# Optimization experiments

Measured on AMD Instinct MI355X. Metric: run time of the kernel, lower is better.

The kernel has to match this reference:

```python
import jax, jax.numpy as jnp
import numpy as np


def setup_inputs() -> dict:
    key = jax.random.key(0)
    k1, k2, k3, k4 = jax.random.split(key, 4)
    return {
        "hidden_states": jax.random.normal(k1, (9, 16, 2048, 768), dtype=jnp.float32),
        "input_ids": jax.random.randint(k2, (16, 2048), 0, 512),
        "layer_logits": jax.random.normal(k3, (8,), dtype=jnp.float32) * 0.02,
        "W": jax.random.normal(k4, (4, 768), dtype=jnp.float32) * 0.02,
        "hte_token_id": 5,
        "d_token_ids": jnp.arange(3),
        "window": 4,
    }


def reference(hidden_states, input_ids, layer_logits, W, hte_token_id, d_token_ids, window):
    # hidden_states: (L+1, B, T, H); drop the embedding layer like the torch code
    layers = hidden_states[1:]              # (L, B, T, H)
    L, B, T, H = layers.shape
    C = W.shape[0]                          # num_heads
    ids = input_ids                         # (B, T)
    wl = jax.nn.softmax(layer_logits)       # (L,) layer mixture weights

    def masked_pool(sel, mask):
        # sel: (L, B, P, H), mask: (B, P) valid-token mask
        scores = jnp.einsum('lbph,ch->lbpc', sel, W)
        scores = jnp.where(mask[None, :, :, None], scores, -jnp.inf)
        attn = jax.nn.softmax(scores, axis=2)          # softmax over tokens P
        pooled = jnp.einsum('lbph,lbpc->lbch', sel, attn)
        return jnp.einsum('l,lbch->bch', wl, pooled).reshape(B, C * H)

    # --- HTE window pooling: first occurrence of hte_token_id, window tokens after ---
    is_hte = ids == hte_token_id
    pos = jnp.where(is_hte.any(axis=1), jnp.argmax(is_hte, axis=1), T - 1)  # (B,)
    offs = jnp.arange(window + 1)
    widx = pos[:, None] + offs              # (B, window+1)
    wvalid = widx < T
    widx = jnp.clip(widx, 0, T - 1)
    sel = layers[:, jnp.arange(B)[:, None], widx]      # (L, B, window+1, H)
    hte_feat = masked_pool(sel, wvalid)

    # --- descriptor pooling: all positions whose id is in d_token_ids ---
    # (masked softmax over full T is math-identical to index_select + softmax,
    #  since softmax-weighted sum is permutation invariant and masked weights are 0)
    dmask = jnp.isin(ids, d_token_ids)      # (B, T)
    dmask = jnp.where(dmask.any(axis=1)[:, None], dmask, jnp.arange(T)[None, :] == 0)
    desc_feat = masked_pool(layers, dmask)

    return jnp.concatenate([hte_feat, desc_feat], axis=-1)  # (B, 2*C*H)
```

## Files before the change

kernel.cpp:

```cpp
#include <hip/hip_runtime.h>
#include <hip/hip_bf16.h>
#include <math.h>


#define CMAX 8
#define KMAX 4

__global__ void mha_scan(const int* __restrict__ ids, const int* __restrict__ hte_id_p,
                         const int* __restrict__ dtok, int nD, int T,
                         int* __restrict__ pos_out, int* __restrict__ nd_out,
                         int* __restrict__ dlist) {
    int b = blockIdx.x;
    __shared__ int s_pos, s_cnt;
    if (threadIdx.x == 0) { s_pos = 0x7fffffff; s_cnt = 0; }
    __syncthreads();
    const int hte = hte_id_p[0];
    const int* row = ids + (size_t)b * T;
    for (int t = threadIdx.x; t < T; t += blockDim.x) {
        int id = row[t];
        if (id == hte) atomicMin(&s_pos, t);
        bool isd = false;
        for (int j = 0; j < nD; ++j) isd |= (id == dtok[j]);
        if (isd) {
            int slot = atomicAdd(&s_cnt, 1);
            dlist[(size_t)b * T + slot] = t;
        }
    }
    __syncthreads();
    if (threadIdx.x == 0) {
        pos_out[b] = (s_pos == 0x7fffffff) ? (T - 1) : s_pos;
        if (s_cnt == 0) { dlist[(size_t)b * T] = 0; nd_out[b] = 1; }
        else nd_out[b] = s_cnt;
    }
}

__global__ void mha_pool(const float* __restrict__ hs, const float* __restrict__ logits,
                         const float* __restrict__ W, const int* __restrict__ win_p,
                         const int* __restrict__ pos_in, const int* __restrict__ nd_in,
                         const int* __restrict__ dlist,
                         int L, int B, int T, int H, int C,
                         float* __restrict__ partial) {
    extern __shared__ float smem[];
    float* lds_W   = smem;
    float* lds_sc  = lds_W + (size_t)C * H;
    float* lds_ms  = lds_sc + (size_t)T * C;
    int*   lds_pos = (int*)(lds_ms + 2 * C);

    const int bx   = blockIdx.x;
    const int part = bx / (L * B);
    const int rem  = bx % (L * B);
    const int l    = rem / B;
    const int b    = rem % B;
    const int tid  = threadIdx.x;
    const int lane = tid & 63;
    const int wave = tid >> 6;
    const int nwaves = blockDim.x >> 6;

    for (int i = tid; i < C * H; i += blockDim.x) lds_W[i] = W[i];

    int npos, p0 = 0;
    if (part == 0) {
        npos = win_p[0] + 1;
        p0 = pos_in[b];
        for (int p = tid; p < npos; p += blockDim.x) {
            int t = p0 + p;
            lds_pos[p] = (t < T) ? t : (T - 1);
        }
    } else {
        npos = nd_in[b];
        for (int p = tid; p < npos; p += blockDim.x)
            lds_pos[p] = dlist[(size_t)b * T + p];
    }
    __syncthreads();

    const float* base = hs + ((size_t)(l + 1) * B + b) * (size_t)T * H;

    for (int p = wave; p < npos; p += nwaves) {
        int t = lds_pos[p];
        bool valid = (part != 0) || (p0 + p < T);
        const float* v = base + (size_t)t * H;
        float s[CMAX];
        #pragma unroll
        for (int c = 0; c < CMAX; ++c) s[c] = 0.f;
        for (int h = lane; h < H; h += 64) {
            float x = v[h];
            for (int c = 0; c < C; ++c) s[c] += x * lds_W[c * H + h];
        }
        for (int c = 0; c < C; ++c) {
            float r = s[c];
            for (int off = 32; off > 0; off >>= 1) r += __shfl_down(r, off);
            if (lane == 0) lds_sc[p * C + c] = valid ? r : -1e30f;
        }
    }
    __syncthreads();

    for (int c = wave; c < C; c += nwaves) {
        float m = -1e30f;
        for (int p = lane; p < npos; p += 64) m = fmaxf(m, lds_sc[p * C + c]);
        for (int off = 32; off > 0; off >>= 1) m = fmaxf(m, __shfl_xor(m, off));
        float sum = 0.f;
        for (int p = lane; p < npos; p += 64) sum += expf(lds_sc[p * C + c] - m);
        for (int off = 32; off > 0; off >>= 1) sum += __shfl_xor(sum, off);
        if (lane == 0) { lds_ms[c] = m; lds_ms[C + c] = sum; }
    }
    __syncthreads();
    for (int i = tid; i < npos * C; i += blockDim.x) {
        int c = i % C;
        lds_sc[i] = expf(lds_sc[i] - lds_ms[c]) / lds_ms[C + c];
    }
    __syncthreads();

    const int K = (H + blockDim.x - 1) / blockDim.x;
    float acc[CMAX][KMAX];
    #pragma unroll
    for (int c = 0; c < CMAX; ++c)
        #pragma unroll
        for (int k = 0; k < KMAX; ++k) acc[c][k] = 0.f;

    for (int p = 0; p < npos; ++p) {
        int t = lds_pos[p];
        const float* v = base + (size_t)t * H;
        float a[CMAX];
        for (int c = 0; c < C; ++c) a[c] = lds_sc[p * C + c];
        for (int k = 0; k < K; ++k) {
            int h = tid + k * blockDim.x;
            if (h < H) {
                float x = v[h];
                for (int c = 0; c < C; ++c) acc[c][k] += a[c] * x;
            }
        }
    }

    float mL = -1e30f;
    for (int i = 0; i < L; ++i) mL = fmaxf(mL, logits[i]);
    float sL = 0.f;
    for (int i = 0; i < L; ++i) sL += expf(logits[i] - mL);
    float wl = expf(logits[l] - mL) / sL;

    float* outp = partial + ((size_t)(part * L + l) * B + b) * ((size_t)C * H);
    for (int k = 0; k < K; ++k) {
        int h = tid + k * blockDim.x;
        if (h < H)
            for (int c = 0; c < C; ++c) outp[c * H + h] = wl * acc[c][k];
    }
}

__global__ void mha_combine(const float* __restrict__ partial, float* __restrict__ out,
                            int L, int B, int CH, int n) {
    int idx = blockIdx.x * blockDim.x + threadIdx.x;
    if (idx >= n) return;
    int b    = idx / (2 * CH);
    int r    = idx % (2 * CH);
    int part = r / CH;
    int ch   = r % CH;
    float s = 0.f;
    for (int l = 0; l < L; ++l)
        s += partial[((size_t)(part * L + l) * B + b) * (size_t)CH + ch];
    out[idx] = s;
}

extern "C" void kernel_launch(void* const* d_in, const int* in_sizes, int n_in,
                              void* d_out, int out_size, void* d_ws, size_t ws_size,
                              hipStream_t stream) {
    const float* hs     = (const float*)d_in[0];
    const int*   ids    = (const int*)d_in[1];
    const float* logits = (const float*)d_in[2];
    const float* W      = (const float*)d_in[3];
    const int*   hte_id = (const int*)d_in[4];
    const int*   dtok   = (const int*)d_in[5];
    const int*   win    = (const int*)d_in[6];

    const int L  = in_sizes[2];
    const int CH = in_sizes[3];
    const int BT = in_sizes[1];
    const int B  = out_size / (2 * CH);
    const int T  = BT / B;
    const long long total = (long long)in_sizes[0];
    const int H  = (int)(total / ((long long)(L + 1) * BT));
    const int C  = CH / H;
    const int nD = in_sizes[5];

    char* ws = (char*)d_ws;
    int* pos   = (int*)ws;
    int* nd    = pos + B;
    int* dlist = nd + B;
    uintptr_t poff = (uintptr_t)(dlist + (size_t)B * T);
    poff = (poff + 15) & ~(uintptr_t)15;
    float* partial = (float*)poff;

    mha_scan<<<B, 256, 0, stream>>>(ids, hte_id, dtok, nD, T, pos, nd, dlist);

    size_t smem = ((size_t)C * H + (size_t)T * C + 2 * C) * sizeof(float)
                + (size_t)T * sizeof(int);
    mha_pool<<<2 * L * B, 256, smem, stream>>>(hs, logits, W, win, pos, nd, dlist,
                                               L, B, T, H, C, partial);

    mha_combine<<<(out_size + 255) / 256, 256, 0, stream>>>(partial, (float*)d_out,
                                                            L, B, CH, out_size);
}
```

Before: 1.048 ms.

## Fuse token scan and layer combine into templated pooling kernel with atomics

Removes the separate scan kernel by having each pooling block rescan its batch row of token ids into LDS. It also drops the combine kernel: each block atomically adds its layer-weighted result into a pre-zeroed output. The score loop now uses float4 loads, and C and K are compile-time template parameters so loops fully unroll. In exchange, every block redundantly scans the ids row, and float atomics make the summation order nondeterministic.

```diff
diff --git a/kernel.cpp b/kernel.cpp
--- a/kernel.cpp
+++ b/kernel.cpp
@@ -6,45 +6,24 @@
 #define CMAX 8
 #define KMAX 4
 
-__global__ void mha_scan(const int* __restrict__ ids, const int* __restrict__ hte_id_p,
-                         const int* __restrict__ dtok, int nD, int T,
-                         int* __restrict__ pos_out, int* __restrict__ nd_out,
-                         int* __restrict__ dlist) {
-    int b = blockIdx.x;
-    __shared__ int s_pos, s_cnt;
-    if (threadIdx.x == 0) { s_pos = 0x7fffffff; s_cnt = 0; }
-    __syncthreads();
-    const int hte = hte_id_p[0];
-    const int* row = ids + (size_t)b * T;
-    for (int t = threadIdx.x; t < T; t += blockDim.x) {
-        int id = row[t];
-        if (id == hte) atomicMin(&s_pos, t);
-        bool isd = false;
-        for (int j = 0; j < nD; ++j) isd |= (id == dtok[j]);
-        if (isd) {
-            int slot = atomicAdd(&s_cnt, 1);
-            dlist[(size_t)b * T + slot] = t;
-        }
-    }
-    __syncthreads();
-    if (threadIdx.x == 0) {
-        pos_out[b] = (s_pos == 0x7fffffff) ? (T - 1) : s_pos;
-        if (s_cnt == 0) { dlist[(size_t)b * T] = 0; nd_out[b] = 1; }
-        else nd_out[b] = s_cnt;
-    }
+__global__ void mha_zero(float* __restrict__ out, int n) {
+    int i = blockIdx.x * blockDim.x + threadIdx.x;
+    if (i < n) out[i] = 0.f;
 }
 
-__global__ void mha_pool(const float* __restrict__ hs, const float* __restrict__ logits,
-                         const float* __restrict__ W, const int* __restrict__ win_p,
-                         const int* __restrict__ pos_in, const int* __restrict__ nd_in,
-                         const int* __restrict__ dlist,
-                         int L, int B, int T, int H, int C,
-                         float* __restrict__ partial) {
+template <int C, int K>
+__global__ void mha_fused(const float* __restrict__ hs, const float* __restrict__ logits,
+                          const float* __restrict__ W, const int* __restrict__ ids,
+                          const int* __restrict__ hte_p, const int* __restrict__ dtok,
+                          int nD, const int* __restrict__ win_p,
+                          int L, int B, int T, int H,
+                          float* __restrict__ out) {
     extern __shared__ float smem[];
     float* lds_W   = smem;
     float* lds_sc  = lds_W + (size_t)C * H;
     float* lds_ms  = lds_sc + (size_t)T * C;
     int*   lds_pos = (int*)(lds_ms + 2 * C);
+    __shared__ int s_pos, s_cnt;
 
     const int bx   = blockIdx.x;
     const int part = bx / (L * B);
@@ -56,39 +35,63 @@
     const int wave = tid >> 6;
     const int nwaves = blockDim.x >> 6;
 
+    if (tid == 0) { s_pos = 0x7fffffff; s_cnt = 0; }
     for (int i = tid; i < C * H; i += blockDim.x) lds_W[i] = W[i];
+    __syncthreads();
+
+    const int hte = hte_p[0];
+    const int* row = ids + (size_t)b * T;
+    for (int t = tid; t < T; t += blockDim.x) {
+        int id = row[t];
+        if (id == hte) atomicMin(&s_pos, t);
+        if (part == 1) {
+            bool isd = false;
+            for (int j = 0; j < nD; ++j) isd |= (id == dtok[j]);
+            if (isd) {
+                int slot = atomicAdd(&s_cnt, 1);
+                lds_pos[slot] = t;
+            }
+        }
+    }
+    __syncthreads();
 
     int npos, p0 = 0;
     if (part == 0) {
         npos = win_p[0] + 1;
-        p0 = pos_in[b];
+        p0 = (s_pos == 0x7fffffff) ? (T - 1) : s_pos;
         for (int p = tid; p < npos; p += blockDim.x) {
             int t = p0 + p;
             lds_pos[p] = (t < T) ? t : (T - 1);
         }
     } else {
-        npos = nd_in[b];
-        for (int p = tid; p < npos; p += blockDim.x)
-            lds_pos[p] = dlist[(size_t)b * T + p];
+        npos = s_cnt;
+        if (npos == 0) { if (tid == 0) lds_pos[0] = 0; npos = 1; }
     }
     __syncthreads();
 
     const float* base = hs + ((size_t)(l + 1) * B + b) * (size_t)T * H;
 
+    const int H4 = H >> 2;
+    const float4* lds_W4 = (const float4*)lds_W;
     for (int p = wave; p < npos; p += nwaves) {
         int t = lds_pos[p];
         bool valid = (part != 0) || (p0 + p < T);
-        const float* v = base + (size_t)t * H;
-        float s[CMAX];
-        #pragma unroll
-        for (int c = 0; c < CMAX; ++c) s[c] = 0.f;
-        for (int h = lane; h < H; h += 64) {
-            float x = v[h];
-            for (int c = 0; c < C; ++c) s[c] += x * lds_W[c * H + h];
-        }
+        const float4* v = (const float4*)(base + (size_t)t * H);
+        float s[C];
+        #pragma unroll
+        for (int c = 0; c < C; ++c) s[c] = 0.f;
+        for (int i = lane; i < H4; i += 64) {
+            float4 x = v[i];
+            #pragma unroll
+            for (int c = 0; c < C; ++c) {
+                float4 w = lds_W4[c * H4 + i];
+                s[c] += x.x * w.x + x.y * w.y + x.z * w.z + x.w * w.w;
+            }
+        }
+        #pragma unroll
         for (int c = 0; c < C; ++c) {
             float r = s[c];
-            for (int off = 32; off > 0; off >>= 1) r += __shfl_down(r, off);
+            for (int off = 32; off > 0; off >>= 1) r += __shfl_xor(r, off);
             if (lane == 0) lds_sc[p * C + c] = valid ? r : -1e30f;
         }
     }
@@ -110,22 +113,24 @@
     }
     __syncthreads();
 
-    const int K = (H + blockDim.x - 1) / blockDim.x;
-    float acc[CMAX][KMAX];
+    float acc[C][K];
     #pragma unroll
-    for (int c = 0; c < CMAX; ++c)
-        #pragma unroll
-        for (int k = 0; k < KMAX; ++k) acc[c][k] = 0.f;
+    for (int c = 0; c < C; ++c)
+        #pragma unroll
+        for (int k = 0; k < K; ++k) acc[c][k] = 0.f;
 
     for (int p = 0; p < npos; ++p) {
         int t = lds_pos[p];
         const float* v = base + (size_t)t * H;
-        float a[CMAX];
+        float a[C];
+        #pragma unroll
         for (int c = 0; c < C; ++c) a[c] = lds_sc[p * C + c];
+        #pragma unroll
         for (int k = 0; k < K; ++k) {
             int h = tid + k * blockDim.x;
             if (h < H) {
                 float x = v[h];
+                #pragma unroll
                 for (int c = 0; c < C; ++c) acc[c][k] += a[c] * x;
             }
         }
@@ -137,26 +142,118 @@
     for (int i = 0; i < L; ++i) sL += expf(logits[i] - mL);
     float wl = expf(logits[l] - mL) / sL;
 
-    float* outp = partial + ((size_t)(part * L + l) * B + b) * ((size_t)C * H);
+    float* outp = out + (size_t)b * (2 * C * H) + (size_t)part * C * H;
+    #pragma unroll
     for (int k = 0; k < K; ++k) {
         int h = tid + k * blockDim.x;
         if (h < H)
-            for (int c = 0; c < C; ++c) outp[c * H + h] = wl * acc[c][k];
+            #pragma unroll
+            for (int c = 0; c < C; ++c)
+                atomicAdd(&outp[c * H + h], wl * acc[c][k]);
     }
 }
 
-__global__ void mha_combine(const float* __restrict__ partial, float* __restrict__ out,
-                            int L, int B, int CH, int n) {
-    int idx = blockIdx.x * blockDim.x + threadIdx.x;
-    if (idx >= n) return;
-    int b    = idx / (2 * CH);
-    int r    = idx % (2 * CH);
-    int part = r / CH;
-    int ch   = r % CH;
-    float s = 0.f;
-    for (int l = 0; l < L; ++l)
-        s += partial[((size_t)(part * L + l) * B + b) * (size_t)CH + ch];
-    out[idx] = s;
+__global__ void mha_fused_gen(const float* __restrict__ hs, const float* __restrict__ logits,
+                              const float* __restrict__ W, const int* __restrict__ ids,
+                              const int* __restrict__ hte_p, const int* __restrict__ dtok,
+                              int nD, const int* __restrict__ win_p,
+                              int L, int B, int T, int H, int C,
+                              float* __restrict__ out) {
+    extern __shared__ float smem[];
+    float* lds_W   = smem;
+    float* lds_sc  = lds_W + (size_t)C * H;
+    float* lds_ms  = lds_sc + (size_t)T * C;
+    int*   lds_pos = (int*)(lds_ms + 2 * C);
+    __shared__ int s_pos, s_cnt;
+
+    const int bx   = blockIdx.x;
+    const int part = bx / (L * B);
+    const int rem  = bx % (L * B);
+    const int l    = rem / B;
+    const int b    = rem % B;
+    const int tid  = threadIdx.x;
+    const int lane = tid & 63;
+    const int wave = tid >> 6;
+    const int nwaves = blockDim.x >> 6;
+
+    if (tid == 0) { s_pos = 0x7fffffff; s_cnt = 0; }
+    for (int i = tid; i < C * H; i += blockDim.x) lds_W[i] = W[i];
+    __syncthreads();
+
+    const int hte = hte_p[0];
+    const int* row = ids + (size_t)b * T;
+    for (int t = tid; t < T; t += blockDim.x) {
+        int id = row[t];
+        if (id == hte) atomicMin(&s_pos, t);
+        if (part == 1) {
+            bool isd = false;
+            for (int j = 0; j < nD; ++j) isd |= (id == dtok[j]);
+            if (isd) lds_pos[atomicAdd(&s_cnt, 1)] = t;
+        }
+    }
+    __syncthreads();
+
+    int npos, p0 = 0;
+    if (part == 0) {
+        npos = win_p[0] + 1;
+        p0 = (s_pos == 0x7fffffff) ? (T - 1) : s_pos;
+        for (int p = tid; p < npos; p += blockDim.x) {
+            int t = p0 + p;
+            lds_pos[p] = (t < T) ? t : (T - 1);
+        }
+    } else {
+        npos = s_cnt;
+        if (npos == 0) { if (tid == 0) lds_pos[0] = 0; npos = 1; }
+    }
+    __syncthreads();
+
+    const float* base = hs + ((size_t)(l + 1) * B + b) * (size_t)T * H;
+
+    for (int pc = wave * C; pc < npos * C; pc += nwaves * C) {
+        int p = pc / C;
+        int t = lds_pos[p];
+        bool valid = (part != 0) || (p0 + p < T);
+        const float* v = base + (size_t)t * H;
+        for (int c = 0; c < C; ++c) {
+            float s = 0.f;
+            for (int h = lane; h < H; h += 64) s += v[h] * lds_W[c * H + h];
+            for (int off = 32; off > 0; off >>= 1) s += __shfl_xor(s, off);
+            if (lane == 0) lds_sc[p * C + c] = valid ? s : -1e30f;
+        }
+    }
+    __syncthreads();
+
+    for (int c = wave; c < C; c += nwaves) {
+        float m = -1e30f;
+        for (int p = lane; p < npos; p += 64) m = fmaxf(m, lds_sc[p * C + c]);
+        for (int off = 32; off > 0; off >>= 1) m = fmaxf(m, __shfl_xor(m, off));
+        float sum = 0.f;
+        for (int p = lane; p < npos; p += 64) sum += expf(lds_sc[p * C + c] - m);
+        for (int off = 32; off > 0; off >>= 1) sum += __shfl_xor(sum, off);
+        if (lane == 0) { lds_ms[c] = m; lds_ms[C + c] = sum; }
+    }
+    __syncthreads();
+    for (int i = tid; i < npos * C; i += blockDim.x) {
+        int c = i % C;
+        lds_sc[i] = expf(lds_sc[i] - lds_ms[c]) / lds_ms[C + c];
+    }
+    __syncthreads();
+
+    float mL = -1e30f;
+    for (int i = 0; i < L; ++i) mL = fmaxf(mL, logits[i]);
+    float sL = 0.f;
+    for (int i = 0; i < L; ++i) sL += expf(logits[i] - mL);
+    float wl = expf(logits[l] - mL) / sL;
+
+    float* outp = out + (size_t)b * (2 * C * H) + (size_t)part * C * H;
+    for (int h = tid; h < H; h += blockDim.x) {
+        for (int c = 0; c < C; ++c) {
+            float acc = 0.f;
+            for (int p = 0; p < npos; ++p)
+                acc += lds_sc[p * C + c] * base[(size_t)lds_pos[p] * H + h];
+            atomicAdd(&outp[c * H + h], wl * acc);
+        }
+    }
 }
 
 extern "C" void kernel_launch(void* const* d_in, const int* in_sizes, int n_in,
@@ -180,21 +277,31 @@
     const int C  = CH / H;
     const int nD = in_sizes[5];
 
-    char* ws = (char*)d_ws;
-    int* pos   = (int*)ws;
-    int* nd    = pos + B;
-    int* dlist = nd + B;
-    uintptr_t poff = (uintptr_t)(dlist + (size_t)B * T);
-    poff = (poff + 15) & ~(uintptr_t)15;
-    float* partial = (float*)poff;
-
-    mha_scan<<<B, 256, 0, stream>>>(ids, hte_id, dtok, nD, T, pos, nd, dlist);
+    float* out = (float*)d_out;
+    mha_zero<<<(out_size + 255) / 256, 256, 0, stream>>>(out, out_size);
 
     size_t smem = ((size_t)C * H + (size_t)T * C + 2 * C) * sizeof(float)
                 + (size_t)T * sizeof(int);
-    mha_pool<<<2 * L * B, 256, smem, stream>>>(hs, logits, W, win, pos, nd, dlist,
-                                               L, B, T, H, C, partial);
-
-    mha_combine<<<(out_size + 255) / 256, 256, 0, stream>>>(partial, (float*)d_out,
-                                                            L, B, CH, out_size);
+    const int grid = 2 * L * B;
+    const int K = (H + 255) / 256;
+
+    if (C == 4 && K == 3 && (H % 4) == 0) {
+        mha_fused<4, 3><<<grid, 256, smem, stream>>>(hs, logits, W, ids, hte_id, dtok,
+                                                     nD, win, L, B, T, H, out);
+    } else if (C == 4 && K == 2 && (H % 4) == 0) {
+        mha_fused<4, 2><<<grid, 256, smem, stream>>>(hs, logits, W, ids, hte_id, dtok,
+                                                     nD, win, L, B, T, H, out);
+    } else if (C == 4 && K == 4 && (H % 4) == 0) {
+        mha_fused<4, 4><<<grid, 256, smem, stream>>>(hs, logits, W, ids, hte_id, dtok,
+                                                     nD, win, L, B, T, H, out);
+    } else if (C == 2 && K == 3 && (H % 4) == 0) {
+        mha_fused<2, 3><<<grid, 256, smem, stream>>>(hs, logits, W, ids, hte_id, dtok,
+                                                     nD, win, L, B, T, H, out);
+    } else if (C == 8 && K == 3 && (H % 4) == 0) {
+        mha_fused<8, 3><<<grid, 256, smem, stream>>>(hs, logits, W, ids, hte_id, dtok,
+                                                     nD, win, L, B, T, H, out);
+    } else {
+        mha_fused_gen<<<grid, 256, smem, stream>>>(hs, logits, W, ids, hte_id, dtok,
+                                                   nD, win, L, B, T, H, C, out);
+    }
 }
```

Measured after the change: 979.3 us. 1.07x faster.
